# Optimization experiments

Measured on AMD Instinct MI355X. Metric: run time of the kernel, lower is better.

Reference implementation:

```python
import jax, jax.numpy as jnp
import numpy as np

B, T, C, HEAD = 4, 4096, 1024, 64
SCALE = 1.0 / (C ** 0.5)  # module divides by embedding_size**0.5, not head_size**0.5


def setup_inputs() -> dict:
    key = jax.random.key(0)
    kx, kq, kk, kv = jax.random.split(key, 4)
    x = jax.random.normal(kx, (B, T, C), dtype=jnp.float32)
    # nn.Linear(C, head_size, bias=False) weights, stored as (C, head_size) for x @ W
    Wq = jax.random.normal(kq, (C, HEAD), dtype=jnp.float32) * (1.0 / np.sqrt(C))
    Wk = jax.random.normal(kk, (C, HEAD), dtype=jnp.float32) * (1.0 / np.sqrt(C))
    Wv = jax.random.normal(kv, (C, HEAD), dtype=jnp.float32) * (1.0 / np.sqrt(C))
    return {"x": x, "Wq": Wq, "Wk": Wk, "Wv": Wv}


def reference(x, Wq, Wk, Wv):
    q = jnp.einsum('btc,ch->bth', x, Wq)  # [B,T,HEAD]
    k = jnp.einsum('btc,ch->bth', x, Wk)
    v = jnp.einsum('btc,ch->bth', x, Wv)
    aff = jnp.einsum('bqh,bkh->bqk', q, k) * SCALE  # [B,T,T]
    causal = jnp.tril(jnp.ones((T, T), dtype=bool))
    aff = jnp.where(causal, aff, -jnp.inf)
    p = jax.nn.softmax(aff, axis=-1)  # dropout p=0.0 -> identity
    return jnp.einsum('bqk,bkh->bqh', p, v)  # [B,T,HEAD]
```

## Files before the change

kernel.cpp:

```cpp
#include <hip/hip_runtime.h>

#define T_SEQ 4096
#define NBATCH 4
#define CDIM 1024
#define NHEAD 64
#define SCALE (1.0f / 32.0f)
#define LOG2E 1.4426950408889634f
#define BT (NBATCH * T_SEQ)
#define NW 8
#define WREG 8960
#define PSTR 17
#define THR2 11.0f

typedef __bf16 bf16x8 __attribute__((ext_vector_type(8)));
typedef float f32x4 __attribute__((ext_vector_type(4)));
typedef unsigned long long u64;

__device__ __forceinline__ unsigned short f2bf(float f) {
  union { float f; unsigned u; } x;
  x.f = f;
  unsigned r = x.u + 0x7FFFu + ((x.u >> 16) & 1u);
  return (unsigned short)(r >> 16);
}

__device__ __forceinline__ unsigned cvt_pk(float lo, float hi) {
  unsigned d;
  asm("v_cvt_pk_bf16_f32 %0, %1, %2" : "=v"(d) : "v"(lo), "v"(hi));
  return d;
}

__device__ __forceinline__ f32x4 mfma16(bf16x8 a, bf16x8 b, f32x4 c) {
  return __builtin_amdgcn_mfma_f32_16x16x32_bf16(a, b, c, 0, 0, 0);
}

__device__ __forceinline__ bf16x8 ones8() {
  bf16x8 v;
  for (int j = 0; j < 8; ++j) v[j] = (__bf16)1.0f;
  return v;
}

__global__ void prep_w(const float* __restrict__ Wq, const float* __restrict__ Wk,
                       const float* __restrict__ Wv, unsigned short* __restrict__ Wt) {
  int c = blockIdx.x;
  const float* W = (c < 64) ? Wq : (c < 128) ? Wk : Wv;
  int cc = c & 63;
  float sc = (c < 64) ? (SCALE * LOG2E) : 1.0f;
  for (int k = threadIdx.x; k < CDIM; k += blockDim.x)
    Wt[c * CDIM + k] = f2bf(W[k * NHEAD + cc] * sc);
}

__global__ __launch_bounds__(256) void proj_qkv(
    const float* __restrict__ x, const unsigned short* __restrict__ Wt,
    unsigned short* __restrict__ qws, unsigned short* __restrict__ kws,
    unsigned short* __restrict__ vtws) {
  __shared__ unsigned short xlds[32][136];
  const int tid = threadIdx.x;
  const int lane = tid & 63;
  const int w = tid >> 6;
  const int g = lane >> 4;
  const int c15 = lane & 15;
  const int rb = blockIdx.x * 32;

  f32x4 acc[2][3];
  for (int i = 0; i < 2; i++)
    for (int j = 0; j < 3; j++) acc[i][j] = (f32x4){0.f, 0.f, 0.f, 0.f};

  const int sr = tid >> 3;
  const int scc = (tid & 7) * 16;
  const float* xrow = x + (size_t)(rb + sr) * CDIM + scc;

  float4 cur[4];
  for (int i = 0; i < 4; i++) cur[i] = *(const float4*)(xrow + i * 4);

  for (int k0 = 0; k0 < CDIM; k0 += 128) {
    unsigned short pk[16];
    for (int i = 0; i < 4; i++) {
      pk[i * 4 + 0] = f2bf(cur[i].x);
      pk[i * 4 + 1] = f2bf(cur[i].y);
      pk[i * 4 + 2] = f2bf(cur[i].z);
      pk[i * 4 + 3] = f2bf(cur[i].w);
    }
    *(bf16x8*)&xlds[sr][scc] = *(bf16x8*)&pk[0];
    *(bf16x8*)&xlds[sr][scc + 8] = *(bf16x8*)&pk[8];
    __syncthreads();
    if (k0 + 128 < CDIM)
      for (int i = 0; i < 4; i++)
        cur[i] = *(const float4*)(xrow + k0 + 128 + i * 4);

    for (int kk = 0; kk < 4; kk++) {
      bf16x8 a[2];
      for (int mt = 0; mt < 2; mt++)
        a[mt] = *(bf16x8*)&xlds[mt * 16 + c15][kk * 32 + g * 8];
      for (int bn = 0; bn < 3; bn++) {
        int col = w * 48 + bn * 16 + c15;
        bf16x8 bfrag =
            *(const bf16x8*)&Wt[(size_t)col * CDIM + k0 + kk * 32 + g * 8];
        for (int mt = 0; mt < 2; mt++)
          acc[mt][bn] = mfma16(a[mt], bfrag, acc[mt][bn]);
      }
    }
    __syncthreads();
  }

  for (int mt = 0; mt < 2; mt++)
    for (int bn = 0; bn < 3; bn++) {
      int col = w * 48 + bn * 16 + c15;
      int row0 = rb + mt * 16 + 4 * g;
      for (int r = 0; r < 4; r++) {
        unsigned short v = f2bf(acc[mt][bn][r]);
        int t = row0 + r;
        if (col < 64)
          qws[(size_t)t * 64 + col] = v;
        else if (col < 128)
          kws[(size_t)t * 64 + (col - 64)] = v;
        else
          vtws[(size_t)(col - 128) * BT + t] = v;
      }
    }
}

__global__ __launch_bounds__(512, 2) void attn_fwd(
    const unsigned short* __restrict__ qws, const unsigned short* __restrict__ kws,
    const unsigned short* __restrict__ vtws, float* __restrict__ out) {
  __shared__ __align__(16) char smem[NW * WREG];
  const int tid = threadIdx.x;
  const int lane = tid & 63;
  const int w = tid >> 6;
  const int g = lane >> 4;
  const int c = lane & 15;
  const int b = blockIdx.x >> 6;
  const int pi = blockIdx.x & 63;
  const size_t rowbase = (size_t)b * T_SEQ;
  char* wbase = smem + w * WREG;
  u64* pl = (u64*)wbase;
  const bf16x8 vone = ones8();

  for (int half = 0; half < 2; ++half) {
    const int qt = half ? (127 - pi) : pi;
    const int qb = qt * 32;
    const int nsteps = (qb >> 6) + 1;

    bf16x8 qf[2][2];
    for (int mi = 0; mi < 2; mi++)
      for (int hc = 0; hc < 2; hc++)
        qf[mi][hc] = *(const bf16x8*)&qws[(rowbase + qb + mi * 16 + c) * 64 +
                                          hc * 32 + g * 8];

    f32x4 o[2][4];
    f32x4 o5[2];
    float mrow[2];
    for (int mi = 0; mi < 2; mi++) {
      for (int nt = 0; nt < 4; nt++) o[mi][nt] = (f32x4){0.f, 0.f, 0.f, 0.f};
      o5[mi] = (f32x4){0.f, 0.f, 0.f, 0.f};
      mrow[mi] = -1e30f;
    }

    for (int st = w; st < nsteps; st += NW) {
      const int kt = st * 64;
      bf16x8 kc0[4], kc1[4], vc[2][4];
      for (int kn = 0; kn < 4; kn++) {
        kc0[kn] = *(const bf16x8*)&kws[(rowbase + kt + kn * 16 + c) * 64 + g * 8];
        kc1[kn] =
            *(const bf16x8*)&kws[(rowbase + kt + kn * 16 + c) * 64 + 32 + g * 8];
      }
      for (int ks = 0; ks < 2; ks++)
        for (int nt = 0; nt < 4; nt++)
          vc[ks][nt] = *(const bf16x8*)&vtws[(size_t)(nt * 16 + c) * BT + rowbase +
                                             kt + ks * 32 + g * 8];

      f32x4 sv[2][4];
      for (int mi = 0; mi < 2; mi++)
        for (int kn = 0; kn < 4; kn++) {
          f32x4 z = (f32x4){0.f, 0.f, 0.f, 0.f};
          z = mfma16(kc0[kn], qf[mi][0], z);
          sv[mi][kn] = mfma16(kc1[kn], qf[mi][1], z);
        }

      if (st == nsteps - 1) {
        for (int mi = 0; mi < 2; mi++)
          for (int kn = 0; kn < 4; kn++)
            for (int r = 0; r < 4; r++) {
              int key = kt + kn * 16 + 4 * g + r;
              int qr = qb + mi * 16 + c;
              if (key > qr) sv[mi][kn][r] = -1e30f;
            }
      }

      for (int mi = 0; mi < 2; mi++) {
        float t0 = fmaxf(fmaxf(sv[mi][0][0], sv[mi][0][1]),
                         fmaxf(sv[mi][0][2], sv[mi][0][3]));
        float t1 = fmaxf(fmaxf(sv[mi][1][0], sv[mi][1][1]),
                         fmaxf(sv[mi][1][2], sv[mi][1][3]));
        float t2 = fmaxf(fmaxf(sv[mi][2][0], sv[mi][2][1]),
                         fmaxf(sv[mi][2][2], sv[mi][2][3]));
        float t3 = fmaxf(fmaxf(sv[mi][3][0], sv[mi][3][1]),
                         fmaxf(sv[mi][3][2], sv[mi][3][3]));
        float t = fmaxf(fmaxf(t0, t1), fmaxf(t2, t3));
        t = fmaxf(t, __shfl_xor(t, 16));
        t = fmaxf(t, __shfl_xor(t, 32));
        if (__any(t > mrow[mi] + THR2)) {
          float mn = fmaxf(mrow[mi], t);
          float a = exp2f(mrow[mi] - mn);
          mrow[mi] = mn;
          for (int nt = 0; nt < 4; nt++) o[mi][nt] *= a;
          o5[mi] *= a;
        }
        int row = mi * 16 + c;
        for (int kn = 0; kn < 4; kn++) {
          float p0 = exp2f(sv[mi][kn][0] - mrow[mi]);
          float p1 = exp2f(sv[mi][kn][1] - mrow[mi]);
          float p2 = exp2f(sv[mi][kn][2] - mrow[mi]);
          float p3 = exp2f(sv[mi][kn][3] - mrow[mi]);
          unsigned dlo = cvt_pk(p0, p1);
          unsigned dhi = cvt_pk(p2, p3);
          pl[row * PSTR + kn * 4 + g] = ((u64)dhi << 32) | dlo;
        }
      }

      asm volatile("" ::: "memory");

      for (int mi = 0; mi < 2; mi++) {
        int row = mi * 16 + c;
        for (int ks = 0; ks < 2; ks++) {
          union { u64 q[2]; bf16x8 v8; } pu;
          pu.q[0] = pl[row * PSTR + ks * 8 + 2 * g];
          pu.q[1] = pl[row * PSTR + ks * 8 + 2 * g + 1];
          bf16x8 pa = pu.v8;
          for (int nt = 0; nt < 4; nt++)
            o[mi][nt] = mfma16(vc[ks][nt], pa, o[mi][nt]);
          o5[mi] = mfma16(vone, pa, o5[mi]);
        }
      }
    }

    float* ow = (float*)wbase;
    float* mw = (float*)(wbase + 8704);
    float* lw = (float*)(wbase + 8832);
    for (int mi = 0; mi < 2; mi++)
      for (int nt = 0; nt < 4; nt++)
        for (int r = 0; r < 4; r++)
          ow[(mi * 16 + c) * 68 + nt * 16 + 4 * g + r] = o[mi][nt][r];
    if (g == 0)
      for (int mi = 0; mi < 2; mi++) {
        mw[mi * 16 + c] = mrow[mi];
        lw[mi * 16 + c] = o5[mi][0];
      }
    __syncthreads();

    for (int i = 0; i < 4; i++) {
      int e = tid + i * 512;
      int row = e >> 6;
      int d = e & 63;
      float M = -1e30f;
      for (int ww = 0; ww < NW; ww++)
        M = fmaxf(M, ((const float*)(smem + ww * WREG + 8704))[row]);
      float L = 0.f, O = 0.f;
      for (int ww = 0; ww < NW; ww++) {
        float mv = ((const float*)(smem + ww * WREG + 8704))[row];
        float f = exp2f(mv - M);
        L += f * ((const float*)(smem + ww * WREG + 8832))[row];
        O += f * ((const float*)(smem + ww * WREG))[row * 68 + d];
      }
      out[(rowbase + qb + row) * 64 + d] = O / L;
    }
    __syncthreads();
  }
}

extern "C" void kernel_launch(void* const* d_in, const int* in_sizes, int n_in,
                              void* d_out, int out_size, void* d_ws, size_t ws_size,
                              hipStream_t stream) {
  const float* x = (const float*)d_in[0];
  const float* Wq = (const float*)d_in[1];
  const float* Wk = (const float*)d_in[2];
  const float* Wv = (const float*)d_in[3];
  float* out = (float*)d_out;

  char* ws = (char*)d_ws;
  unsigned short* Wt = (unsigned short*)(ws);
  unsigned short* qws = (unsigned short*)(ws + 393216);
  unsigned short* kws = (unsigned short*)(ws + 393216 + 2097152);
  unsigned short* vtws = (unsigned short*)(ws + 393216 + 2 * 2097152);

  prep_w<<<dim3(192), dim3(256), 0, stream>>>(Wq, Wk, Wv, Wt);
  proj_qkv<<<dim3(512), dim3(256), 0, stream>>>(x, Wt, qws, kws, vtws);
  attn_fwd<<<dim3(256), dim3(512), 0, stream>>>(qws, kws, vtws, out);
}
```

Measured before the change: 80.49 us.

## Switch attention inner loop to 32x32x16 MFMA with register-shuffled P

Rewrites the attention key loop to use 32x32x16 bf16 MFMA with 32-key steps instead of 16x16x32 tiles over 64 keys. The P matrix is now rebuilt in registers with cross-half lane shuffles rather than a round trip through LDS. The row sum is accumulated with scalar adds instead of an extra MFMA against a ones vector. It also preloads all W fragments per k-chunk in the projection kernel before issuing MFMAs. The finer key steps double the loop iterations, and the larger accumulators may add register pressure.

```diff
diff --git a/kernel.cpp b/kernel.cpp
--- a/kernel.cpp
+++ b/kernel.cpp
@@ -9,11 +9,11 @@
 #define BT (NBATCH * T_SEQ)
 #define NW 8
 #define WREG 8960
-#define PSTR 17
 #define THR2 11.0f
 
 typedef __bf16 bf16x8 __attribute__((ext_vector_type(8)));
 typedef float f32x4 __attribute__((ext_vector_type(4)));
+typedef float f32x16 __attribute__((ext_vector_type(16)));
 typedef unsigned long long u64;
 
 __device__ __forceinline__ unsigned short f2bf(float f) {
@@ -33,10 +33,8 @@
   return __builtin_amdgcn_mfma_f32_16x16x32_bf16(a, b, c, 0, 0, 0);
 }
 
-__device__ __forceinline__ bf16x8 ones8() {
-  bf16x8 v;
-  for (int j = 0; j < 8; ++j) v[j] = (__bf16)1.0f;
-  return v;
+__device__ __forceinline__ f32x16 mfma32(bf16x8 a, bf16x8 b, f32x16 c) {
+  return __builtin_amdgcn_mfma_f32_32x32x16_bf16(a, b, c, 0, 0, 0);
 }
 
 __global__ void prep_w(const float* __restrict__ Wq, const float* __restrict__ Wk,
@@ -87,17 +85,21 @@
       for (int i = 0; i < 4; i++)
         cur[i] = *(const float4*)(xrow + k0 + 128 + i * 4);
 
+    bf16x8 wfrag[4][3];
+    for (int kk = 0; kk < 4; kk++)
+      for (int bn = 0; bn < 3; bn++) {
+        int col = w * 48 + bn * 16 + c15;
+        wfrag[kk][bn] =
+            *(const bf16x8*)&Wt[(size_t)col * CDIM + k0 + kk * 32 + g * 8];
+      }
+
     for (int kk = 0; kk < 4; kk++) {
       bf16x8 a[2];
       for (int mt = 0; mt < 2; mt++)
         a[mt] = *(bf16x8*)&xlds[mt * 16 + c15][kk * 32 + g * 8];
-      for (int bn = 0; bn < 3; bn++) {
-        int col = w * 48 + bn * 16 + c15;
-        bf16x8 bfrag =
-            *(const bf16x8*)&Wt[(size_t)col * CDIM + k0 + kk * 32 + g * 8];
+      for (int bn = 0; bn < 3; bn++)
         for (int mt = 0; mt < 2; mt++)
-          acc[mt][bn] = mfma16(a[mt], bfrag, acc[mt][bn]);
-      }
+          acc[mt][bn] = mfma16(a[mt], wfrag[kk][bn], acc[mt][bn]);
     }
     __syncthreads();
   }
@@ -126,125 +128,107 @@
   const int tid = threadIdx.x;
   const int lane = tid & 63;
   const int w = tid >> 6;
-  const int g = lane >> 4;
-  const int c = lane & 15;
+  const int q31 = lane & 31;
+  const int hi = lane >> 5;
   const int b = blockIdx.x >> 6;
   const int pi = blockIdx.x & 63;
   const size_t rowbase = (size_t)b * T_SEQ;
   char* wbase = smem + w * WREG;
-  u64* pl = (u64*)wbase;
-  const bf16x8 vone = ones8();
 
   for (int half = 0; half < 2; ++half) {
     const int qt = half ? (127 - pi) : pi;
     const int qb = qt * 32;
-    const int nsteps = (qb >> 6) + 1;
-
-    bf16x8 qf[2][2];
-    for (int mi = 0; mi < 2; mi++)
-      for (int hc = 0; hc < 2; hc++)
-        qf[mi][hc] = *(const bf16x8*)&qws[(rowbase + qb + mi * 16 + c) * 64 +
-                                          hc * 32 + g * 8];
-
-    f32x4 o[2][4];
-    f32x4 o5[2];
-    float mrow[2];
-    for (int mi = 0; mi < 2; mi++) {
-      for (int nt = 0; nt < 4; nt++) o[mi][nt] = (f32x4){0.f, 0.f, 0.f, 0.f};
-      o5[mi] = (f32x4){0.f, 0.f, 0.f, 0.f};
-      mrow[mi] = -1e30f;
-    }
+    const int nsteps = qt + 1;
+
+    bf16x8 qf[4];
+    for (int h2 = 0; h2 < 4; h2++)
+      qf[h2] = *(const bf16x8*)&qws[(rowbase + qb + q31) * 64 + h2 * 16 + hi * 8];
+
+    f32x16 o[2];
+    o[0] = (f32x16)0.f;
+    o[1] = (f32x16)0.f;
+    float mrow = -1e30f;
+    float lrun = 0.f;
 
     for (int st = w; st < nsteps; st += NW) {
-      const int kt = st * 64;
-      bf16x8 kc0[4], kc1[4], vc[2][4];
-      for (int kn = 0; kn < 4; kn++) {
-        kc0[kn] = *(const bf16x8*)&kws[(rowbase + kt + kn * 16 + c) * 64 + g * 8];
-        kc1[kn] =
-            *(const bf16x8*)&kws[(rowbase + kt + kn * 16 + c) * 64 + 32 + g * 8];
-      }
-      for (int ks = 0; ks < 2; ks++)
-        for (int nt = 0; nt < 4; nt++)
-          vc[ks][nt] = *(const bf16x8*)&vtws[(size_t)(nt * 16 + c) * BT + rowbase +
-                                             kt + ks * 32 + g * 8];
-
-      f32x4 sv[2][4];
-      for (int mi = 0; mi < 2; mi++)
-        for (int kn = 0; kn < 4; kn++) {
-          f32x4 z = (f32x4){0.f, 0.f, 0.f, 0.f};
-          z = mfma16(kc0[kn], qf[mi][0], z);
-          sv[mi][kn] = mfma16(kc1[kn], qf[mi][1], z);
+      const int kt = st * 32;
+      bf16x8 ka[4];
+      for (int h2 = 0; h2 < 4; h2++)
+        ka[h2] =
+            *(const bf16x8*)&kws[(rowbase + kt + q31) * 64 + h2 * 16 + hi * 8];
+      bf16x8 va[2][2];
+      for (int nt = 0; nt < 2; nt++)
+        for (int ki = 0; ki < 2; ki++)
+          va[nt][ki] = *(const bf16x8*)&vtws[(size_t)(nt * 32 + q31) * BT +
+                                             rowbase + kt + ki * 16 + hi * 8];
+
+      f32x16 s = (f32x16)0.f;
+      for (int h2 = 0; h2 < 4; h2++) s = mfma32(ka[h2], qf[h2], s);
+
+      float sv[16];
+      for (int r = 0; r < 16; r++) sv[r] = s[r];
+
+      if (st == nsteps - 1) {
+        for (int r = 0; r < 16; r++) {
+          int key = kt + (r & 3) + 8 * (r >> 2) + 4 * hi;
+          if (key > qb + q31) sv[r] = -1e30f;
         }
-
-      if (st == nsteps - 1) {
-        for (int mi = 0; mi < 2; mi++)
-          for (int kn = 0; kn < 4; kn++)
-            for (int r = 0; r < 4; r++) {
-              int key = kt + kn * 16 + 4 * g + r;
-              int qr = qb + mi * 16 + c;
-              if (key > qr) sv[mi][kn][r] = -1e30f;
-            }
-      }
-
-      for (int mi = 0; mi < 2; mi++) {
-        float t0 = fmaxf(fmaxf(sv[mi][0][0], sv[mi][0][1]),
-                         fmaxf(sv[mi][0][2], sv[mi][0][3]));
-        float t1 = fmaxf(fmaxf(sv[mi][1][0], sv[mi][1][1]),
-                         fmaxf(sv[mi][1][2], sv[mi][1][3]));
-        float t2 = fmaxf(fmaxf(sv[mi][2][0], sv[mi][2][1]),
-                         fmaxf(sv[mi][2][2], sv[mi][2][3]));
-        float t3 = fmaxf(fmaxf(sv[mi][3][0], sv[mi][3][1]),
-                         fmaxf(sv[mi][3][2], sv[mi][3][3]));
-        float t = fmaxf(fmaxf(t0, t1), fmaxf(t2, t3));
-        t = fmaxf(t, __shfl_xor(t, 16));
-        t = fmaxf(t, __shfl_xor(t, 32));
-        if (__any(t > mrow[mi] + THR2)) {
-          float mn = fmaxf(mrow[mi], t);
-          float a = exp2f(mrow[mi] - mn);
-          mrow[mi] = mn;
-          for (int nt = 0; nt < 4; nt++) o[mi][nt] *= a;
-          o5[mi] *= a;
-        }
-        int row = mi * 16 + c;
-        for (int kn = 0; kn < 4; kn++) {
-          float p0 = exp2f(sv[mi][kn][0] - mrow[mi]);
-          float p1 = exp2f(sv[mi][kn][1] - mrow[mi]);
-          float p2 = exp2f(sv[mi][kn][2] - mrow[mi]);
-          float p3 = exp2f(sv[mi][kn][3] - mrow[mi]);
-          unsigned dlo = cvt_pk(p0, p1);
-          unsigned dhi = cvt_pk(p2, p3);
-          pl[row * PSTR + kn * 4 + g] = ((u64)dhi << 32) | dlo;
-        }
-      }
-
-      asm volatile("" ::: "memory");
-
-      for (int mi = 0; mi < 2; mi++) {
-        int row = mi * 16 + c;
-        for (int ks = 0; ks < 2; ks++) {
-          union { u64 q[2]; bf16x8 v8; } pu;
-          pu.q[0] = pl[row * PSTR + ks * 8 + 2 * g];
-          pu.q[1] = pl[row * PSTR + ks * 8 + 2 * g + 1];
-          bf16x8 pa = pu.v8;
-          for (int nt = 0; nt < 4; nt++)
-            o[mi][nt] = mfma16(vc[ks][nt], pa, o[mi][nt]);
-          o5[mi] = mfma16(vone, pa, o5[mi]);
-        }
+      }
+
+      float t01 = fmaxf(sv[0], sv[1]), t23 = fmaxf(sv[2], sv[3]);
+      float t45 = fmaxf(sv[4], sv[5]), t67 = fmaxf(sv[6], sv[7]);
+      float t89 = fmaxf(sv[8], sv[9]), tab = fmaxf(sv[10], sv[11]);
+      float tcd = fmaxf(sv[12], sv[13]), tef = fmaxf(sv[14], sv[15]);
+      float t = fmaxf(fmaxf(fmaxf(t01, t23), fmaxf(t45, t67)),
+                      fmaxf(fmaxf(t89, tab), fmaxf(tcd, tef)));
+      t = fmaxf(t, __shfl_xor(t, 32));
+      if (__any(t > mrow + THR2)) {
+        float mn = fmaxf(mrow, t);
+        float a = exp2f(mrow - mn);
+        mrow = mn;
+        o[0] *= a;
+        o[1] *= a;
+        lrun *= a;
+      }
+      float p[16];
+      for (int r = 0; r < 16; r++) p[r] = exp2f(sv[r] - mrow);
+
+      float ssum = 0.f;
+      for (int r = 0; r < 16; r++) ssum += p[r];
+      lrun += ssum + __shfl_xor(ssum, 32);
+
+      unsigned X[8], Y[8];
+      for (int j = 0; j < 8; j++) X[j] = cvt_pk(p[2 * j], p[2 * j + 1]);
+      for (int j = 0; j < 8; j++) Y[j] = __shfl_xor(X[j], 32);
+
+      union { unsigned u[4]; bf16x8 v; } bf0, bf1;
+      bf0.u[0] = hi ? Y[2] : X[0];
+      bf0.u[1] = hi ? Y[3] : X[1];
+      bf0.u[2] = hi ? X[2] : Y[0];
+      bf0.u[3] = hi ? X[3] : Y[1];
+      bf1.u[0] = hi ? Y[6] : X[4];
+      bf1.u[1] = hi ? Y[7] : X[5];
+      bf1.u[2] = hi ? X[6] : Y[4];
+      bf1.u[3] = hi ? X[7] : Y[5];
+
+      for (int nt = 0; nt < 2; nt++) {
+        o[nt] = mfma32(va[nt][0], bf0.v, o[nt]);
+        o[nt] = mfma32(va[nt][1], bf1.v, o[nt]);
       }
     }
 
     float* ow = (float*)wbase;
     float* mw = (float*)(wbase + 8704);
     float* lw = (float*)(wbase + 8832);
-    for (int mi = 0; mi < 2; mi++)
-      for (int nt = 0; nt < 4; nt++)
-        for (int r = 0; r < 4; r++)
-          ow[(mi * 16 + c) * 68 + nt * 16 + 4 * g + r] = o[mi][nt][r];
-    if (g == 0)
-      for (int mi = 0; mi < 2; mi++) {
-        mw[mi * 16 + c] = mrow[mi];
-        lw[mi * 16 + c] = o5[mi][0];
-      }
+    for (int nt = 0; nt < 2; nt++)
+      for (int r = 0; r < 16; r++) {
+        int d = nt * 32 + (r & 3) + 8 * (r >> 2) + 4 * hi;
+        ow[q31 * 68 + d] = o[nt][r];
+      }
+    if (hi == 0) {
+      mw[q31] = mrow;
+      lw[q31] = lrun;
+    }
     __syncthreads();
 
     for (int i = 0; i < 4; i++) {
```

Result: no change. 79.65 us (-1.0%).
